# Optimization experiments

Hardware: AMD Instinct MI355X
Metric: run time of the kernel (lower is better)

## Reference

```python
import jax, jax.numpy as jnp
import numpy as np

B, S, HID = 4, 2048, 2048
H, HKV, D = 16, 4, 128
RANK = 512
SCALE = D ** -0.5


def setup_inputs() -> dict:
    key = jax.random.key(0)
    ks = jax.random.split(key, 5)
    scale_w = 0.02
    return {
        "hidden_states": jax.random.normal(ks[0], (B, S, HID), dtype=jnp.float32),
        "Wq": jax.random.normal(ks[1], (HID, H * D), dtype=jnp.float32) * scale_w,
        "Wc": jax.random.normal(ks[2], (HID, RANK), dtype=jnp.float32) * scale_w,
        "Wup": jax.random.normal(ks[3], (RANK, HKV * D), dtype=jnp.float32) * scale_w,
        "Wo": jax.random.normal(ks[4], (H * D, HID), dtype=jnp.float32) * scale_w,
    }


def reference(hidden_states, Wq, Wc, Wup, Wo):
    b, s, _ = hidden_states.shape
    n_rep = H // HKV
    # Q projection -> (b, H, s, D)
    q = (hidden_states @ Wq).reshape(b, s, H, D).transpose(0, 2, 1, 3)
    # low-rank KV compression -> (b, s, RANK)
    kv_c = hidden_states @ Wc
    # gate in source is ones -> sigmoid(1) constant scalar multiply
    kv_c = kv_c * jax.nn.sigmoid(jnp.float32(1.0))
    # decompress: single kv_up_proj produces shared K/V content
    kv = (kv_c @ Wup).reshape(b, s, HKV, D).transpose(0, 2, 1, 3)  # (b, HKV, s, D)
    k = jnp.repeat(kv, n_rep, axis=1)  # (b, H, s, D), repeat_interleave over heads
    v = k
    scores = jnp.einsum("bhqd,bhkd->bhqk", q, k) * SCALE
    attn = jax.nn.softmax(scores.astype(jnp.float32), axis=-1).astype(q.dtype)
    out = jnp.einsum("bhqk,bhkd->bhqd", attn, v)
    out = out.transpose(0, 2, 1, 3).reshape(b, s, H * D)
    return out @ Wo
```

## Files before the change

kernel.cpp:

```cpp
#include <hip/hip_runtime.h>
#include <hip/hip_bf16.h>
#include <stdint.h>

#define DEV __device__ __forceinline__

typedef __bf16 bf16x8 __attribute__((ext_vector_type(8)));
typedef float f32x4 __attribute__((ext_vector_type(4)));
typedef float f32x16 __attribute__((ext_vector_type(16)));
typedef int i32x4 __attribute__((ext_vector_type(4)));


DEV void gload_lds16(const void* g, void* l) {
  __builtin_amdgcn_global_load_lds((const __attribute__((address_space(1))) void*)g,
                                   (__attribute__((address_space(3))) void*)l, 16, 0, 0);
}

__global__ __launch_bounds__(256) void k_cast(const float* __restrict__ in,
                                              __hip_bfloat16* __restrict__ out, int n) {
  int i = (blockIdx.x * 256 + threadIdx.x) * 8;
  if (i >= n) return;
  const float4* p = (const float4*)(in + i);
  float4 a = p[0], c = p[1];
  bf16x8 v;
  v[0] = (__bf16)a.x; v[1] = (__bf16)a.y; v[2] = (__bf16)a.z; v[3] = (__bf16)a.w;
  v[4] = (__bf16)c.x; v[5] = (__bf16)c.y; v[6] = (__bf16)c.z; v[7] = (__bf16)c.w;
  *(bf16x8*)(out + i) = v;
}

__global__ __launch_bounds__(256) void k_tcast(const float* __restrict__ in,
                                               __hip_bfloat16* __restrict__ out, int R, int C) {
  __shared__ float t[32][33];
  int c0 = blockIdx.x * 32, r0 = blockIdx.y * 32;
  int x = threadIdx.x, y0 = threadIdx.y;
  for (int j = y0; j < 32; j += 8) t[j][x] = in[(size_t)(r0 + j) * C + c0 + x];
  __syncthreads();
  for (int j = y0; j < 32; j += 8)
    out[(size_t)(c0 + j) * R + r0 + x] = __float2bfloat16(t[x][j]);
}

__global__ __launch_bounds__(256) void k_tbf16(const __hip_bfloat16* __restrict__ in,
                                               __hip_bfloat16* __restrict__ out) {
  __shared__ unsigned short t[32][33];
  int z = blockIdx.z;
  const unsigned short* ip = (const unsigned short*)in + (size_t)z * 2048 * 128;
  unsigned short* op = (unsigned short*)out + (size_t)z * 2048 * 128;
  int d0 = blockIdx.x * 32, s0 = blockIdx.y * 32;
  int x = threadIdx.x, y0 = threadIdx.y;
  for (int j = y0; j < 32; j += 8) t[j][x] = ip[(size_t)(s0 + j) * 128 + d0 + x];
  __syncthreads();
  for (int j = y0; j < 32; j += 8) op[(size_t)(d0 + j) * 2048 + s0 + x] = t[x][j];
}

template <int MODE>
__global__ __launch_bounds__(256, 2) void k_gemm(const __hip_bfloat16* __restrict__ A,
                                                 const __hip_bfloat16* __restrict__ BT,
                                                 void* __restrict__ Cout,
                                                 int M, int N, int K, float scale) {
  __shared__ __align__(16) __hip_bfloat16 As[128 * 64];
  __shared__ __align__(16) __hip_bfloat16 Bs[128 * 64];
  const int tid = threadIdx.x;
  const int lane = tid & 63, wid = tid >> 6;
  const int g = lane >> 4, lr = lane & 15;
  const int m0 = blockIdx.x * 128, n0 = blockIdx.y * 128;
  const int wr = wid >> 1, wc = wid & 1;
  const f32x4 vzero = {0.f, 0.f, 0.f, 0.f};

  f32x4 acc[4][4];
#pragma unroll
  for (int i = 0; i < 4; ++i)
#pragma unroll
    for (int j = 0; j < 4; ++j) acc[i][j] = vzero;

  const char* aSrc[4];
  const char* bSrc[4];
  char* aDst[4];
  char* bDst[4];
#pragma unroll
  for (int i = 0; i < 4; ++i) {
    int p = i * 4096 + tid * 16;
    int row = p >> 7, colb = p & 127;
    int scol = colb ^ ((row & 7) << 4);
    aSrc[i] = (const char*)A + ((size_t)(m0 + row) * K) * 2 + scol;
    bSrc[i] = (const char*)BT + ((size_t)(n0 + row) * K) * 2 + scol;
    aDst[i] = (char*)As + i * 4096 + wid * 1024;
    bDst[i] = (char*)Bs + i * 4096 + wid * 1024;
  }

  const int nk = K >> 6;
  for (int kt = 0; kt < nk; ++kt) {
    const size_t ko = (size_t)kt * 128;
#pragma unroll
    for (int i = 0; i < 4; ++i) gload_lds16(aSrc[i] + ko, aDst[i]);
#pragma unroll
    for (int i = 0; i < 4; ++i) gload_lds16(bSrc[i] + ko, bDst[i]);
    __syncthreads();
#pragma unroll
    for (int kc = 0; kc < 2; ++kc) {
      bf16x8 af[4], bfr[4];
#pragma unroll
      for (int fm = 0; fm < 4; ++fm) {
        int row = wr * 64 + fm * 16 + lr;
        int cb = (kc * 64 + g * 16) ^ ((row & 7) << 4);
        af[fm] = *(const bf16x8*)((const char*)As + row * 128 + cb);
      }
#pragma unroll
      for (int fn = 0; fn < 4; ++fn) {
        int row = wc * 64 + fn * 16 + lr;
        int cb = (kc * 64 + g * 16) ^ ((row & 7) << 4);
        bfr[fn] = *(const bf16x8*)((const char*)Bs + row * 128 + cb);
      }
#pragma unroll
      for (int fm = 0; fm < 4; ++fm)
#pragma unroll
        for (int fn = 0; fn < 4; ++fn)
          acc[fm][fn] =
              __builtin_amdgcn_mfma_f32_16x16x32_bf16(af[fm], bfr[fn], acc[fm][fn], 0, 0, 0);
    }
    __syncthreads();
  }

#pragma unroll
  for (int fm = 0; fm < 4; ++fm) {
#pragma unroll
    for (int fn = 0; fn < 4; ++fn) {
      const int mb = m0 + wr * 64 + fm * 16 + g * 4;
      const int n = n0 + wc * 64 + fn * 16 + lr;
#pragma unroll
      for (int r = 0; r < 4; ++r) {
        float v = acc[fm][fn][r] * scale;
        int m = mb + r;
        if constexpr (MODE == 2) {
          int b = m >> 11, s = m & 2047, hk = n >> 7, d = n & 127;
          ((__hip_bfloat16*)Cout)[(((size_t)(b * 4 + hk) * 2048) + s) * 128 + d] =
              __float2bfloat16(v);
        } else {
          ((__hip_bfloat16*)Cout)[(size_t)n * M + m] = __float2bfloat16(v);
        }
      }
    }
  }
}

template <int MODE>
__global__ __launch_bounds__(512, 2) void k_gemm256(const __hip_bfloat16* __restrict__ A,
                                                    const __hip_bfloat16* __restrict__ BT,
                                                    void* __restrict__ Cout,
                                                    int M, int N, int K, float scale) {
  __shared__ __align__(16) char smem[131072];
  const int tid = threadIdx.x;
  const int lane = tid & 63, wid = tid >> 6;
  const int lr = lane & 15, g = lane >> 4;
  const int bid = blockIdx.x;
  const int swz = (bid & 7) * 32 + (bid >> 3);
  const int m0 = (swz & 31) * 256, n0 = (swz >> 5) * 256;
  const int wr = wid >> 2, wc = wid & 3;
  const size_t K2 = (size_t)K * 2;
  const f32x4 vzero = {0.f, 0.f, 0.f, 0.f};

  const int srow = tid >> 3, sslot = tid & 7;
  const int sw = (sslot ^ (srow & 7)) << 4;
  const char* gA = (const char*)A + (size_t)(m0 + srow) * K2 + sw;
  const char* gB = (const char*)BT + (size_t)(n0 + srow) * K2 + sw;
  const size_t hG = (size_t)128 * K2;
  const size_t r2 = (size_t)64 * K2;
  char* const ldsW = smem + wid * 1024;

  auto stage = [&](int buf, int half, int isB, size_t koB) {
    const char* src = (isB ? gB : gA) + (half ? hG : 0) + koB;
    char* dst = ldsW + buf * 65536 + isB * 32768 + half * 16384;
    gload_lds16(src, dst);
    gload_lds16(src + r2, dst + 8192);
  };

  const int sl0 = ((0 + g) ^ (lr & 7)) << 4;
  const int sl1 = ((4 + g) ^ (lr & 7)) << 4;
  const char* aB = smem + (wr * 64 + lr) * 128;
  const char* bB = smem + 32768 + (wc * 32 + lr) * 128;

  f32x4 acc[8][4];
#pragma unroll
  for (int i = 0; i < 8; ++i)
#pragma unroll
    for (int j = 0; j < 4; ++j) acc[i][j] = vzero;

  bf16x8 a[4][2], bl[2][2], bh[2][2];
  auto ldA = [&](int buf, int half) {
    const char* p = aB + buf * 65536 + half * 16384;
#pragma unroll
    for (int f = 0; f < 4; ++f) {
      a[f][0] = *(const bf16x8*)(p + f * 2048 + sl0);
      a[f][1] = *(const bf16x8*)(p + f * 2048 + sl1);
    }
  };
  auto ldB = [&](int buf, int half, bf16x8 (&b)[2][2]) {
    const char* p = bB + buf * 65536 + half * 16384;
#pragma unroll
    for (int n = 0; n < 2; ++n) {
      b[n][0] = *(const bf16x8*)(p + n * 2048 + sl0);
      b[n][1] = *(const bf16x8*)(p + n * 2048 + sl1);
    }
  };
  auto mm = [&](bf16x8 (&b)[2][2], int fr, int nc) {
    __builtin_amdgcn_s_setprio(1);
#pragma unroll
    for (int kc = 0; kc < 2; ++kc)
#pragma unroll
      for (int f = 0; f < 4; ++f)
#pragma unroll
        for (int n = 0; n < 2; ++n)
          acc[fr + f][nc + n] = __builtin_amdgcn_mfma_f32_16x16x32_bf16(
              a[f][kc], b[n][kc], acc[fr + f][nc + n], 0, 0, 0);
    __builtin_amdgcn_s_setprio(0);
  };

  auto tile = [&](int buf, size_t koN, bool st) {
    ldA(buf, 0);
    ldB(buf, 0, bl);
    if (st) {
      stage(buf ^ 1, 0, 0, koN);
      asm volatile("s_waitcnt vmcnt(4)" ::: "memory");
    } else {
      asm volatile("s_waitcnt vmcnt(2)" ::: "memory");
    }
    __builtin_amdgcn_s_barrier();
    asm volatile("s_waitcnt lgkmcnt(0)" ::: "memory");
    __builtin_amdgcn_sched_barrier(0);
    mm(bl, 0, 0);
    ldB(buf, 1, bh);
    if (st) {
      stage(buf ^ 1, 0, 1, koN);
      asm volatile("s_waitcnt vmcnt(4)" ::: "memory");
    } else {
      asm volatile("s_waitcnt vmcnt(0)" ::: "memory");
    }
    __builtin_amdgcn_s_barrier();
    asm volatile("s_waitcnt lgkmcnt(0)" ::: "memory");
    __builtin_amdgcn_sched_barrier(0);
    mm(bh, 0, 2);
    ldA(buf, 1);
    if (st) stage(buf ^ 1, 1, 1, koN);
    __builtin_amdgcn_s_barrier();
    asm volatile("s_waitcnt lgkmcnt(0)" ::: "memory");
    __builtin_amdgcn_sched_barrier(0);
    mm(bh, 4, 2);
    if (st) {
      stage(buf ^ 1, 1, 0, koN);
      asm volatile("s_waitcnt vmcnt(4)" ::: "memory");
    }
    __builtin_amdgcn_s_barrier();
    __builtin_amdgcn_sched_barrier(0);
    mm(bl, 4, 0);
  };

  stage(0, 0, 0, 0);
  stage(0, 0, 1, 0);
  stage(0, 1, 1, 0);
  stage(0, 1, 0, 0);
  asm volatile("s_waitcnt vmcnt(4)" ::: "memory");
  __builtin_amdgcn_s_barrier();

  const int nk = K >> 6;
  size_t ko = 128;
#pragma unroll 1
  for (int t = 0; t < nk - 2; t += 2) {
    tile(0, ko, true); ko += 128;
    tile(1, ko, true); ko += 128;
  }
  tile(0, ko, true);
  tile(1, 0, false);

#pragma unroll
  for (int fm = 0; fm < 8; ++fm) {
    const int mrow = m0 + (fm >> 2) * 128 + wr * 64 + (fm & 3) * 16 + g * 4;
#pragma unroll
    for (int fn = 0; fn < 4; ++fn) {
      const int n = n0 + (fn >> 1) * 128 + wc * 32 + (fn & 1) * 16 + lr;
#pragma unroll
      for (int r = 0; r < 4; ++r) {
        float v = acc[fm][fn][r] * scale;
        int m = mrow + r;
        if constexpr (MODE == 0) {
          ((float*)Cout)[(size_t)m * N + n] = v;
        } else {
          int b = m >> 11, s = m & 2047, h = n >> 7, d = n & 127;
          ((__hip_bfloat16*)Cout)[(((size_t)(b * 16 + h) * 2048) + s) * 128 + d] =
              __float2bfloat16(v);
        }
      }
    }
  }
}

__global__ __launch_bounds__(512, 2) void k_attn2(const __hip_bfloat16* __restrict__ q,
                                                  const __hip_bfloat16* __restrict__ kv,
                                                  const __hip_bfloat16* __restrict__ kvT,
                                                  __hip_bfloat16* __restrict__ out) {
  __shared__ __align__(16) char smem[65536];
  const int tid = threadIdx.x, lane = tid & 63, wid = tid >> 6;
  const int hi = lane >> 5, lq = lane & 31;
  const int qt = blockIdx.x;
  const int pair = blockIdx.y;
  const int b = pair >> 2, hkv = pair & 3;
  const int h = hkv * 4 + (wid & 3);
  const int q0w = qt * 64 + (wid >> 2) * 32;

  const char* qrow =
      (const char*)q + (((size_t)(b * 16 + h) * 2048 + q0w + lq) * 128 + hi * 8) * 2;
  bf16x8 qfr[8];
#pragma unroll
  for (int kt = 0; kt < 8; ++kt) qfr[kt] = *(const bf16x8*)(qrow + kt * 32);

  const char* kbase = (const char*)kv + ((size_t)pair * 2048 * 128) * 2;
  const char* tbase = (const char*)kvT + ((size_t)pair * 2048 * 128) * 2;
  const char* pK;
  const char* pV;
  {
    int p0 = tid * 16;
    int krow = p0 >> 8, kcol = p0 & 255;
    pK = kbase + (size_t)krow * 256 + (kcol ^ ((krow & 15) << 4));
    int vrow = p0 >> 7, vcol = p0 & 127;
    pV = tbase + (size_t)vrow * 4096 + (vcol ^ ((vrow & 7) << 4));
  }

  f32x16 accO[4];
#pragma unroll
  for (int dt = 0; dt < 4; ++dt)
#pragma unroll
    for (int i = 0; i < 16; ++i) accO[dt][i] = 0.f;
  float m_run = -1e30f, l_run = 0.f;

  const int hsK = (hi * 16) ^ ((lq & 15) << 4);
  const int hsV = (hi * 16) ^ ((lq & 7) << 4);

  auto stage = [&](int kb, int vb) {
    gload_lds16(pK, smem + kb + wid * 1024);
    gload_lds16(pK + 8192, smem + kb + 8192 + wid * 1024);
    gload_lds16(pV, smem + vb + wid * 1024);
    gload_lds16(pV + 262144, smem + vb + 8192 + wid * 1024);
    pK += 16384;
    pV += 128;
  };

  auto compute = [&](int kb, int vb) {
    f32x16 st[2];
#pragma unroll
    for (int i = 0; i < 16; ++i) { st[0][i] = 0.f; st[1][i] = 0.f; }
    const char* Kb = smem + kb;
#pragma unroll
    for (int tau = 0; tau < 2; ++tau) {
      const char* Kr = Kb + (tau * 32 + lq) * 256;
#pragma unroll
      for (int kt = 0; kt < 8; ++kt) {
        bf16x8 kf = *(const bf16x8*)(Kr + ((kt * 32) ^ hsK));
        st[tau] = __builtin_amdgcn_mfma_f32_32x32x16_bf16(kf, qfr[kt], st[tau], 0, 0, 0);
      }
    }
    float mloc[8];
#pragma unroll
    for (int i = 0; i < 8; ++i)
      mloc[i] = fmaxf(fmaxf(st[0][i], st[0][i + 8]), fmaxf(st[1][i], st[1][i + 8]));
#pragma unroll
    for (int i = 0; i < 4; ++i) mloc[i] = fmaxf(mloc[i], mloc[i + 4]);
    float pm = fmaxf(fmaxf(mloc[0], mloc[1]), fmaxf(mloc[2], mloc[3]));
    pm = fmaxf(pm, __shfl_xor(pm, 32));
    if (__any(pm > m_run + 8.f)) {
      float mnew = fmaxf(m_run, pm);
      float alpha = __builtin_amdgcn_exp2f(m_run - mnew);
      m_run = mnew;
      l_run *= alpha;
#pragma unroll
      for (int dt = 0; dt < 4; ++dt)
#pragma unroll
        for (int i = 0; i < 16; ++i) accO[dt][i] *= alpha;
    }
    float p0[16], p1[16];
#pragma unroll
    for (int i = 0; i < 16; ++i) p0[i] = __builtin_amdgcn_exp2f(st[0][i] - m_run);
#pragma unroll
    for (int i = 0; i < 16; ++i) p1[i] = __builtin_amdgcn_exp2f(st[1][i] - m_run);
    float s0 = 0.f, s1 = 0.f, s2 = 0.f, s3 = 0.f;
#pragma unroll
    for (int i = 0; i < 8; ++i) {
      s0 += p0[i]; s1 += p0[i + 8]; s2 += p1[i]; s3 += p1[i + 8];
    }
    l_run += (s0 + s1) + (s2 + s3);
    bf16x8 pfr[4];
#pragma unroll
    for (int ks = 0; ks < 4; ++ks) {
      const int base = (ks & 1) * 8;
      int A0, A1, B0, B1;
      if (ks < 2) {
        asm("v_cvt_pk_bf16_f32 %0, %1, %2" : "=v"(A0) : "v"(p0[base + 0]), "v"(p0[base + 1]));
        asm("v_cvt_pk_bf16_f32 %0, %1, %2" : "=v"(A1) : "v"(p0[base + 2]), "v"(p0[base + 3]));
        asm("v_cvt_pk_bf16_f32 %0, %1, %2" : "=v"(B0) : "v"(p0[base + 4]), "v"(p0[base + 5]));
        asm("v_cvt_pk_bf16_f32 %0, %1, %2" : "=v"(B1) : "v"(p0[base + 6]), "v"(p0[base + 7]));
      } else {
        asm("v_cvt_pk_bf16_f32 %0, %1, %2" : "=v"(A0) : "v"(p1[base + 0]), "v"(p1[base + 1]));
        asm("v_cvt_pk_bf16_f32 %0, %1, %2" : "=v"(A1) : "v"(p1[base + 2]), "v"(p1[base + 3]));
        asm("v_cvt_pk_bf16_f32 %0, %1, %2" : "=v"(B0) : "v"(p1[base + 4]), "v"(p1[base + 5]));
        asm("v_cvt_pk_bf16_f32 %0, %1, %2" : "=v"(B1) : "v"(p1[base + 6]), "v"(p1[base + 7]));
      }
      asm("v_permlane32_swap_b32 %0, %1" : "+v"(A0), "+v"(B0));
      asm("v_permlane32_swap_b32 %0, %1" : "+v"(A1), "+v"(B1));
      union { int w[4]; bf16x8 v; } u;
      u.w[0] = A0; u.w[1] = A1; u.w[2] = B0; u.w[3] = B1;
      pfr[ks] = u.v;
    }
    const char* Vb = smem + vb;
#pragma unroll
    for (int dt = 0; dt < 4; ++dt) {
      const char* Vr = Vb + (dt * 32 + lq) * 128;
#pragma unroll
      for (int ks = 0; ks < 4; ++ks) {
        bf16x8 vf = *(const bf16x8*)(Vr + ((ks * 32) ^ hsV));
        accO[dt] = __builtin_amdgcn_mfma_f32_32x32x16_bf16(vf, pfr[ks], accO[dt], 0, 0, 0);
      }
    }
  };

  stage(0, 32768);
  __syncthreads();
#pragma unroll 1
  for (int it = 0; it < 16; ++it) {
    stage(16384, 49152);
    compute(0, 32768);
    __syncthreads();
    if (it < 15) stage(0, 32768);
    compute(16384, 49152);
    __syncthreads();
  }

  float lt = l_run + __shfl_xor(l_run, 32);
  float inv = 1.f / lt;
#pragma unroll
  for (int dt = 0; dt < 4; ++dt)
#pragma unroll
    for (int i = 0; i < 16; ++i) accO[dt][i] *= inv;

  __syncthreads();
  char* scr = smem + wid * 8192;
  const int swq = (lq & 15) << 4;
#pragma unroll
  for (int dt = 0; dt < 4; ++dt) {
#pragma unroll
    for (int rp = 0; rp < 8; ++rp) {
      int w;
      asm("v_cvt_pk_bf16_f32 %0, %1, %2"
          : "=v"(w)
          : "v"(accO[dt][2 * rp]), "v"(accO[dt][2 * rp + 1]));
      int dloc = ((2 * rp) & 3) + 8 * (rp >> 1) + 4 * hi;
      int bytec = (dt * 64 + dloc * 2) ^ swq;
      *(int*)(scr + lq * 256 + bytec) = w;
    }
  }
  __syncthreads();
  const int l16 = lane & 15, lh = lane >> 4;
#pragma unroll
  for (int ps = 0; ps < 8; ++ps) {
    int qr = ps * 4 + lh;
    i32x4 v = *(const i32x4*)(scr + qr * 256 + ((l16 * 16) ^ ((qr & 15) << 4)));
    char* dst = (char*)out + (((size_t)(b * 2048 + q0w + qr) * 2048) + h * 128 + l16 * 8) * 2;
    *(i32x4*)dst = v;
  }
}

extern "C" void kernel_launch(void* const* d_in, const int* in_sizes, int n_in,
                              void* d_out, int out_size, void* d_ws, size_t ws_size,
                              hipStream_t stream) {
  const float* hs = (const float*)d_in[0];
  const float* Wq = (const float*)d_in[1];
  const float* Wc = (const float*)d_in[2];
  const float* Wup = (const float*)d_in[3];
  const float* Wo = (const float*)d_in[4];

  if (ws_size < 105381888u) return;
  char* ws = (char*)d_ws;
  __hip_bfloat16* hs_bf = (__hip_bfloat16*)(ws + 0);
  __hip_bfloat16* q_attn = (__hip_bfloat16*)(ws + 33554432);
  __hip_bfloat16* kvb = (__hip_bfloat16*)(ws + 67108864);
  __hip_bfloat16* kvT = (__hip_bfloat16*)(ws + 75497472);
  __hip_bfloat16* WqT = (__hip_bfloat16*)(ws + 83886080);
  __hip_bfloat16* WoT = (__hip_bfloat16*)(ws + 92274688);
  __hip_bfloat16* WupT = (__hip_bfloat16*)(ws + 100663296);
  __hip_bfloat16* Wc_bf = (__hip_bfloat16*)(ws + 101187584);
  __hip_bfloat16* WckvT = (__hip_bfloat16*)(ws + 103284736);
  __hip_bfloat16* attnout = hs_bf;

  const float qscale = (float)(0.08838834764831845 * 1.4426950408889634);

  k_cast<<<8192, 256, 0, stream>>>(hs, hs_bf, 16777216);
  k_cast<<<512, 256, 0, stream>>>(Wc, Wc_bf, 1048576);
  k_tcast<<<dim3(64, 64), dim3(32, 8), 0, stream>>>(Wq, WqT, 2048, 2048);
  k_tcast<<<dim3(64, 64), dim3(32, 8), 0, stream>>>(Wo, WoT, 2048, 2048);
  k_tcast<<<dim3(16, 16), dim3(32, 8), 0, stream>>>(Wup, WupT, 512, 512);
  k_gemm<3><<<dim3(16, 4), 256, 0, stream>>>(Wc_bf, WupT, WckvT, 2048, 512, 512,
                                             0.7310585786300049f);
  k_gemm256<1><<<256, 512, 0, stream>>>(hs_bf, WqT, q_attn, 8192, 2048, 2048, qscale);
  k_gemm<2><<<dim3(64, 4), 256, 0, stream>>>(hs_bf, WckvT, kvb, 8192, 512, 2048, 1.0f);
  k_tbf16<<<dim3(4, 64, 16), dim3(32, 8), 0, stream>>>(kvb, kvT);
  k_attn2<<<dim3(32, 16), 512, 0, stream>>>(q_attn, kvb, kvT, attnout);
  k_gemm256<0><<<256, 512, 0, stream>>>(attnout, WoT, d_out, 8192, 2048, 2048, 1.0f);
}
```

Baseline: 353.5 us.

## Restructure GEMM LDS staging to refill current buffer quarters in-place

Reworks the double-buffered GEMM main loop so that, once a quarter of the current LDS buffer has been consumed, the next-next k-tile's quarter is staged into that same buffer. Only the last quarter goes to the other buffer, which deepens the global-to-LDS prefetch distance. The prologue now preloads seven quarters across both buffers, and vmcnt waits move to the end of each tile. It adds extra s_barriers between consume and overwrite phases to avoid races, at the cost of more synchronisation per tile.

```diff
diff --git a/kernel.cpp b/kernel.cpp
--- a/kernel.cpp
+++ b/kernel.cpp
@@ -165,17 +165,35 @@
   const size_t r2 = (size_t)64 * K2;
   char* const ldsW = smem + wid * 1024;
 
-  auto stage = [&](int buf, int half, int isB, size_t koB) {
-    const char* src = (isB ? gB : gA) + (half ? hG : 0) + koB;
+  auto stageH = [&](int isB, int half, int buf, size_t ko) {
+    const char* src = (isB ? gB : gA) + (half ? hG : 0) + ko;
     char* dst = ldsW + buf * 65536 + isB * 32768 + half * 16384;
     gload_lds16(src, dst);
     gload_lds16(src + r2, dst + 8192);
   };
 
-  const int sl0 = ((0 + g) ^ (lr & 7)) << 4;
-  const int sl1 = ((4 + g) ^ (lr & 7)) << 4;
-  const char* aB = smem + (wr * 64 + lr) * 128;
-  const char* bB = smem + 32768 + (wc * 32 + lr) * 128;
+  const int rowA = (wr * 64 + lr) * 128;
+  const int rowB = (wc * 32 + lr) * 128;
+  const int sl0 = ((0 ^ (lr & 7)) << 4);
+  bf16x8 a[8], b0[4], b1[4];
+  auto ldA = [&](int buf, int mh) {
+    const char* p = smem + buf * 65536 + mh * 16384 + rowA;
+#pragma unroll
+    for (int rb = 0; rb < 4; ++rb)
+#pragma unroll
+      for (int kc = 0; kc < 2; ++kc)
+        a[rb * 2 + kc] =
+            *(const bf16x8*)(p + rb * 2048 + (((kc * 4 + g) ^ (lr & 7)) << 4));
+  };
+  auto ldB = [&](int buf, int nh, bf16x8 (&b)[4]) {
+    const char* p = smem + buf * 65536 + 32768 + nh * 16384 + rowB;
+#pragma unroll
+    for (int rb = 0; rb < 2; ++rb)
+#pragma unroll
+      for (int kc = 0; kc < 2; ++kc)
+        b[rb * 2 + kc] =
+            *(const bf16x8*)(p + rb * 2048 + (((kc * 4 + g) ^ (lr & 7)) << 4));
+  };
 
   f32x4 acc[8][4];
 #pragma unroll
@@ -183,91 +201,70 @@
 #pragma unroll
     for (int j = 0; j < 4; ++j) acc[i][j] = vzero;
 
-  bf16x8 a[4][2], bl[2][2], bh[2][2];
-  auto ldA = [&](int buf, int half) {
-    const char* p = aB + buf * 65536 + half * 16384;
-#pragma unroll
-    for (int f = 0; f < 4; ++f) {
-      a[f][0] = *(const bf16x8*)(p + f * 2048 + sl0);
-      a[f][1] = *(const bf16x8*)(p + f * 2048 + sl1);
-    }
-  };
-  auto ldB = [&](int buf, int half, bf16x8 (&b)[2][2]) {
-    const char* p = bB + buf * 65536 + half * 16384;
-#pragma unroll
-    for (int n = 0; n < 2; ++n) {
-      b[n][0] = *(const bf16x8*)(p + n * 2048 + sl0);
-      b[n][1] = *(const bf16x8*)(p + n * 2048 + sl1);
-    }
-  };
-  auto mm = [&](bf16x8 (&b)[2][2], int fr, int nc) {
+  auto mm = [&](bf16x8 (&b)[4], int fmB, int fnB) {
     __builtin_amdgcn_s_setprio(1);
 #pragma unroll
     for (int kc = 0; kc < 2; ++kc)
 #pragma unroll
-      for (int f = 0; f < 4; ++f)
-#pragma unroll
-        for (int n = 0; n < 2; ++n)
-          acc[fr + f][nc + n] = __builtin_amdgcn_mfma_f32_16x16x32_bf16(
-              a[f][kc], b[n][kc], acc[fr + f][nc + n], 0, 0, 0);
+      for (int rb = 0; rb < 4; ++rb)
+#pragma unroll
+        for (int nb = 0; nb < 2; ++nb)
+          acc[fmB + rb][fnB + nb] = __builtin_amdgcn_mfma_f32_16x16x32_bf16(
+              a[rb * 2 + kc], b[nb * 2 + kc], acc[fmB + rb][fnB + nb], 0, 0, 0);
     __builtin_amdgcn_s_setprio(0);
   };
 
-  auto tile = [&](int buf, size_t koN, bool st) {
+  auto tile = [&](int buf, size_t ko1, size_t ko2, bool s1, bool s2, bool w6, bool w0) {
     ldA(buf, 0);
-    ldB(buf, 0, bl);
-    if (st) {
-      stage(buf ^ 1, 0, 0, koN);
-      asm volatile("s_waitcnt vmcnt(4)" ::: "memory");
-    } else {
-      asm volatile("s_waitcnt vmcnt(2)" ::: "memory");
-    }
+    ldB(buf, 0, b0);
+    if (s1) stageH(0, 1, buf ^ 1, ko1);
+    asm volatile("s_waitcnt lgkmcnt(8)" ::: "memory");
     __builtin_amdgcn_s_barrier();
     asm volatile("s_waitcnt lgkmcnt(0)" ::: "memory");
     __builtin_amdgcn_sched_barrier(0);
-    mm(bl, 0, 0);
-    ldB(buf, 1, bh);
-    if (st) {
-      stage(buf ^ 1, 0, 1, koN);
-      asm volatile("s_waitcnt vmcnt(4)" ::: "memory");
-    } else {
-      asm volatile("s_waitcnt vmcnt(0)" ::: "memory");
-    }
+    mm(b0, 0, 0);
+    __builtin_amdgcn_s_barrier();
+    ldB(buf, 1, b1);
+    if (s2) stageH(0, 0, buf, ko2);
     __builtin_amdgcn_s_barrier();
     asm volatile("s_waitcnt lgkmcnt(0)" ::: "memory");
     __builtin_amdgcn_sched_barrier(0);
-    mm(bh, 0, 2);
+    mm(b1, 0, 2);
+    __builtin_amdgcn_s_barrier();
     ldA(buf, 1);
-    if (st) stage(buf ^ 1, 1, 1, koN);
+    if (s2) stageH(1, 0, buf, ko2);
     __builtin_amdgcn_s_barrier();
     asm volatile("s_waitcnt lgkmcnt(0)" ::: "memory");
     __builtin_amdgcn_sched_barrier(0);
-    mm(bh, 4, 2);
-    if (st) {
-      stage(buf ^ 1, 1, 0, koN);
-      asm volatile("s_waitcnt vmcnt(4)" ::: "memory");
-    }
+    mm(b1, 4, 2);
+    __builtin_amdgcn_s_barrier();
+    if (s2) stageH(1, 1, buf, ko2);
     __builtin_amdgcn_s_barrier();
     __builtin_amdgcn_sched_barrier(0);
-    mm(bl, 4, 0);
-  };
-
-  stage(0, 0, 0, 0);
-  stage(0, 0, 1, 0);
-  stage(0, 1, 1, 0);
-  stage(0, 1, 0, 0);
-  asm volatile("s_waitcnt vmcnt(4)" ::: "memory");
+    mm(b0, 4, 0);
+    if (w6) asm volatile("s_waitcnt vmcnt(6)" ::: "memory");
+    else if (w0) asm volatile("s_waitcnt vmcnt(0)" ::: "memory");
+    __builtin_amdgcn_s_barrier();
+  };
+
+  stageH(0, 0, 0, 0);
+  stageH(1, 0, 0, 0);
+  stageH(1, 1, 0, 0);
+  stageH(0, 1, 0, 0);
+  stageH(0, 0, 1, 128);
+  stageH(1, 0, 1, 128);
+  stageH(1, 1, 1, 128);
+  asm volatile("s_waitcnt vmcnt(6)" ::: "memory");
   __builtin_amdgcn_s_barrier();
 
   const int nk = K >> 6;
-  size_t ko = 128;
 #pragma unroll 1
   for (int t = 0; t < nk - 2; t += 2) {
-    tile(0, ko, true); ko += 128;
-    tile(1, ko, true); ko += 128;
-  }
-  tile(0, ko, true);
-  tile(1, 0, false);
+    tile(0, (size_t)(t + 1) * 128, (size_t)(t + 2) * 128, true, true, true, false);
+    tile(1, (size_t)(t + 2) * 128, (size_t)(t + 3) * 128, true, true, true, false);
+  }
+  tile(0, (size_t)(nk - 1) * 128, 0, true, false, false, true);
+  tile(1, 0, 0, false, false, false, false);
 
 #pragma unroll
   for (int fm = 0; fm < 8; ++fm) {
```

After: 348.4 us. Within noise of the previous version (-1.4%).
